# Performance work log

Measured on AMD Instinct MI355X. Metric: run time of the kernel, lower is better.

Reference implementation:

```python
import jax, jax.numpy as jnp
import numpy as np

BATCH = 8192
IN_FEATURES = 4096
OUT_FEATURES = 4096
TT_RANK = 8
IN_MODES = (16, 16, 16)
OUT_MODES = (16, 16, 16)


def setup_inputs() -> dict:
    key = jax.random.key(0)
    ks = jax.random.split(key, 5)
    # core std ~ glorot-ish scale for TT factors
    std = 0.05
    x = jax.random.normal(ks[0], (BATCH, IN_FEATURES), dtype=jnp.float32)
    core0 = std * jax.random.normal(ks[1], (1, OUT_MODES[0], IN_MODES[0], TT_RANK), dtype=jnp.float32)
    core1 = std * jax.random.normal(ks[2], (TT_RANK, OUT_MODES[1], IN_MODES[1], TT_RANK), dtype=jnp.float32)
    core2 = std * jax.random.normal(ks[3], (TT_RANK, OUT_MODES[2], IN_MODES[2], 1), dtype=jnp.float32)
    bias = 0.001 * jnp.ones((OUT_FEATURES,), dtype=jnp.float32)
    return {"x": x, "core0": core0, "core1": core1, "core2": core2, "bias": bias}


def _tt_dense_matmul(cores, b):
    """A @ b where A (out_features x in_features) is in TT-matrix format.
    cores[k]: (r_k, o_k, i_k, r_{k+1}), r_0 = r_d = 1. b: (in_features, batch).
    Returns (out_features, batch). Mirrors t3nsor/t3f tt_dense_matmul."""
    in_dims = [c.shape[2] for c in cores]
    ranks = [c.shape[0] for c in cores] + [cores[-1].shape[3]]
    out_features = int(np.prod([c.shape[1] for c in cores]))
    data = b.T                                   # (batch, in_features)
    data = data.reshape(-1, in_dims[-1], 1)      # (batch*prod(i[:-1]), i_last, r_d=1)
    for k in range(len(cores) - 1, -1, -1):
        # core (a=r_k, i=o_k, j=i_k, b=r_{k+1}); data (r, j, b) -> (i, r, a)
        data = jnp.einsum('aijb,rjb->ira', cores[k], data)
        if k > 0:
            data = data.reshape(-1, in_dims[k - 1], ranks[k])
    return data.reshape(out_features, -1)        # (out_features, batch)


def reference(x, core0, core1, core2, bias):
    # forward: tt_dense_matmul(weight_t, x^T)^T + bias
    y = _tt_dense_matmul([core0, core1, core2], x.T)  # (out_features, batch)
    return y.T + bias                                 # (batch, out_features)
```

## Files before the change

kernel.cpp:

```cpp
#include <hip/hip_runtime.h>
#include <hip/hip_bf16.h>
#include <cstdint>


typedef __bf16 bf16x8 __attribute__((ext_vector_type(8)));
typedef float f32x4 __attribute__((ext_vector_type(4)));
typedef unsigned short u16;
typedef u16 u16x8 __attribute__((ext_vector_type(8)));

__device__ __forceinline__ u16 f2bf(float f) {
    unsigned u = __builtin_bit_cast(unsigned, f);
    u += 0x7fffu + ((u >> 16) & 1u);
    return (u16)(u >> 16);
}

__global__ void k_cvt(const float* __restrict__ x, u16* __restrict__ xb) {
    long i = (long)blockIdx.x * blockDim.x + threadIdx.x;
    const float4* p = (const float4*)x;
    float4 a = p[2 * i], b = p[2 * i + 1];
    u16x8 o;
    o[0] = f2bf(a.x); o[1] = f2bf(a.y); o[2] = f2bf(a.z); o[3] = f2bf(a.w);
    o[4] = f2bf(b.x); o[5] = f2bf(b.y); o[6] = f2bf(b.z); o[7] = f2bf(b.w);
    ((u16x8*)xb)[i] = o;
}

__global__ void k_c01(const float* __restrict__ c0, const float* __restrict__ c1,
                      float* __restrict__ c01) {
    int idx = blockIdx.x * 256 + threadIdx.x;
    int b2 = idx & 7, i1 = (idx >> 3) & 15, i0 = (idx >> 7) & 15;
    int o1 = (idx >> 11) & 15, o0 = idx >> 15;
    float s = 0.f;
#pragma unroll
    for (int b1 = 0; b1 < 8; ++b1)
        s += c0[(o0 * 16 + i0) * 8 + b1] * c1[((b1 * 16 + o1) * 16 + i1) * 8 + b2];
    c01[idx] = s;
}

__global__ void k_w(const float* __restrict__ c01, const float* __restrict__ c2,
                    u16* __restrict__ wbt) {
    int idx = blockIdx.x * 256 + threadIdx.x;
    int i2h = idx & 1;
    int i1 = (idx >> 1) & 15;
    int i0 = (idx >> 5) & 15;
    int o = idx >> 9;
    int o2 = o & 15, o1 = (o >> 4) & 15, o0 = o >> 8;
    const float* c = &c01[(((o0 * 16 + o1) * 16 + i0) * 16 + i1) * 8];
    float acc[8] = {0, 0, 0, 0, 0, 0, 0, 0};
#pragma unroll
    for (int b2 = 0; b2 < 8; ++b2) {
        float cv = c[b2];
        const float* cc = &c2[(b2 * 16 + o2) * 16 + i2h * 8];
#pragma unroll
        for (int j = 0; j < 8; ++j) acc[j] += cv * cc[j];
    }
    u16x8 ov;
#pragma unroll
    for (int j = 0; j < 8; ++j) ov[j] = f2bf(acc[j]);
    ((u16x8*)wbt)[(long)o * 512 + (i0 * 32 + i1 * 2 + i2h)] = ov;
}

#define GM 128
#define GN 128
#define GK 64

__device__ __forceinline__ void gload_lds16(const void* g, void* l) {
    __builtin_amdgcn_global_load_lds(
        (const __attribute__((address_space(1))) unsigned*)g,
        (__attribute__((address_space(3))) unsigned*)l, 16, 0, 0);
}

__global__ void k_gemm(const u16* __restrict__ A, const u16* __restrict__ B,
                       const float* __restrict__ bias, float* __restrict__ C,
                       int M, int N, int K) {
    __shared__ __align__(16) u16 lA[GM * GK];
    __shared__ __align__(16) u16 lB[GN * GK];
    const int t = threadIdx.x;
    const int m0 = blockIdx.y * GM, n0 = blockIdx.x * GN;
    const int wave = t >> 6, lane = t & 63;
    const int wm = (wave >> 1) * 64, wn = (wave & 1) * 64;
    const int lr = lane & 15, quad = lane >> 4;
    const int sw = lr & 7;

    f32x4 acc[4][4];
#pragma unroll
    for (int mi = 0; mi < 4; ++mi)
#pragma unroll
        for (int ni = 0; ni < 4; ++ni) acc[mi][ni] = 0.f;

    for (int k0 = 0; k0 < K; k0 += GK) {
#pragma unroll
        for (int j = 0; j < 4; ++j) {
            int ci = j * 256 + t;
            int r = ci >> 3;
            int c = (ci & 7) ^ (r & 7);
            gload_lds16(&A[(long)(m0 + r) * K + k0 + c * 8], &lA[ci * 8]);
        }
#pragma unroll
        for (int j = 0; j < 4; ++j) {
            int ci = j * 256 + t;
            int r = ci >> 3;
            int c = (ci & 7) ^ (r & 7);
            gload_lds16(&B[(long)(n0 + r) * K + k0 + c * 8], &lB[ci * 8]);
        }
        __syncthreads();
#pragma unroll
        for (int kk2 = 0; kk2 < 2; ++kk2) {
            const int sl = ((kk2 * 4 + quad) ^ sw) * 8;
            bf16x8 af[4], bfr[4];
#pragma unroll
            for (int i = 0; i < 4; ++i)
                af[i] = *(const bf16x8*)&lA[(wm + i * 16 + lr) * GK + sl];
#pragma unroll
            for (int i = 0; i < 4; ++i)
                bfr[i] = *(const bf16x8*)&lB[(wn + i * 16 + lr) * GK + sl];
#pragma unroll
            for (int mi = 0; mi < 4; ++mi)
#pragma unroll
                for (int ni = 0; ni < 4; ++ni)
                    acc[mi][ni] = __builtin_amdgcn_mfma_f32_16x16x32_bf16(
                        af[mi], bfr[ni], acc[mi][ni], 0, 0, 0);
        }
        __syncthreads();
    }

#pragma unroll
    for (int ni = 0; ni < 4; ++ni) {
        int gn = n0 + wn + ni * 16 + lr;
        float bv = bias[gn];
#pragma unroll
        for (int mi = 0; mi < 4; ++mi) {
            int gm = m0 + wm + mi * 16 + quad * 4;
#pragma unroll
            for (int r = 0; r < 4; ++r)
                C[(long)(gm + r) * N + gn] = acc[mi][ni][r] + bv;
        }
    }
}

extern "C" void kernel_launch(void* const* d_in, const int* in_sizes, int n_in,
                              void* d_out, int out_size, void* d_ws, size_t ws_size,
                              hipStream_t stream) {
    const float* x = (const float*)d_in[0];
    const float* c0 = (const float*)d_in[1];
    const float* c1 = (const float*)d_in[2];
    const float* c2 = (const float*)d_in[3];
    const float* bias = (const float*)d_in[4];
    float* out = (float*)d_out;

    const int Mb = 8192, Nf = 4096, Kf = 4096;
    char* ws = (char*)d_ws;
    u16* xb = (u16*)ws;
    u16* wbt = (u16*)(ws + 67108864);
    float* c01 = (float*)(ws + 67108864 + 33554432);

    k_cvt<<<dim3((Mb * Kf / 8) / 256), 256, 0, stream>>>(x, xb);
    k_c01<<<dim3(2048), 256, 0, stream>>>(c0, c1, c01);
    k_w<<<dim3(8192), 256, 0, stream>>>(c01, c2, wbt);
    k_gemm<<<dim3(Nf / GN, Mb / GM), 256, 0, stream>>>(xb, wbt, bias, out, Mb, Nf, Kf);
}
```

Baseline: 476.4 us.

## Rewrite GEMM with 256x256 tiles, 4-stage LDS ring pipeline and XCD swizzle

Replaces the 128x128 single-buffered GEMM with a 256x256 tile, 8-wave workgroup that streams K in 32-wide slices through a 4-deep LDS ring of async global-to-LDS loads. Prefetches run three tiles ahead, with explicit vmcnt waits, split A/B issue, barriers and s_setprio around MFMA bursts, so that memory latency overlaps compute. A workgroup index swizzle groups tiles to improve L2 reuse. Each workgroup uses 128 KB of dynamic LDS, which limits occupancy and relies on the hand-placed waits and barriers being correct.

```diff
diff --git a/kernel.cpp b/kernel.cpp
--- a/kernel.cpp
+++ b/kernel.cpp
@@ -1,5 +1,4 @@
 #include <hip/hip_runtime.h>
-#include <hip/hip_bf16.h>
 #include <cstdint>
 
 
@@ -59,9 +58,15 @@
     ((u16x8*)wbt)[(long)o * 512 + (i0 * 32 + i1 * 2 + i2h)] = ov;
 }
 
-#define GM 128
-#define GN 128
-#define GK 64
+#define BM 256
+#define BN 256
+#define BK 32
+#define NBUF 4
+#define TA (BM * BK)
+#define TB (BN * BK)
+#define LDS_BYTES (NBUF * (TA + TB) * 2)
+
+static_assert(LDS_BYTES == 131072, "lds size");
 
 __device__ __forceinline__ void gload_lds16(const void* g, void* l) {
     __builtin_amdgcn_global_load_lds(
@@ -69,67 +74,129 @@
         (__attribute__((address_space(3))) unsigned*)l, 16, 0, 0);
 }
 
+__launch_bounds__(512, 2)
 __global__ void k_gemm(const u16* __restrict__ A, const u16* __restrict__ B,
                        const float* __restrict__ bias, float* __restrict__ C,
                        int M, int N, int K) {
-    __shared__ __align__(16) u16 lA[GM * GK];
-    __shared__ __align__(16) u16 lB[GN * GK];
+    extern __shared__ __align__(16) u16 lds[];
+    u16* lA = lds;
+    u16* lB = lds + NBUF * TA;
+
+    const int wg = blockIdx.x;
+    const int swz = (wg & 7) * 64 + (wg >> 3);
+    const int bn = swz & 15, bm = swz >> 4;
+    const int m0 = bm * BM, n0 = bn * BN;
+
     const int t = threadIdx.x;
-    const int m0 = blockIdx.y * GM, n0 = blockIdx.x * GN;
     const int wave = t >> 6, lane = t & 63;
-    const int wm = (wave >> 1) * 64, wn = (wave & 1) * 64;
+    const int wm = wave >> 2, wn = wave & 3;
     const int lr = lane & 15, quad = lane >> 4;
-    const int sw = lr & 7;
-
-    f32x4 acc[4][4];
-#pragma unroll
-    for (int mi = 0; mi < 4; ++mi)
+
+    const u16* pa[2]; const u16* pb[2]; int lof[2];
+#pragma unroll
+    for (int j = 0; j < 2; ++j) {
+        int ci = j * 512 + t;
+        int r = ci >> 2;
+        int c = (ci & 3) ^ ((r >> 1) & 3);
+        pa[j] = &A[(long)(m0 + r) * K + c * 8];
+        pb[j] = &B[(long)(n0 + r) * K + c * 8];
+        lof[j] = ci * 8;
+    }
+
+    int offA[8], offB[4];
+#pragma unroll
+    for (int mi = 0; mi < 8; ++mi) {
+        int r = wm * 128 + mi * 16 + lr;
+        offA[mi] = r * BK + ((quad ^ ((r >> 1) & 3)) << 3);
+    }
+#pragma unroll
+    for (int ni = 0; ni < 4; ++ni) {
+        int r = wn * 64 + ni * 16 + lr;
+        offB[ni] = r * BK + ((quad ^ ((r >> 1) & 3)) << 3);
+    }
+
+    f32x4 acc[8][4];
+#pragma unroll
+    for (int mi = 0; mi < 8; ++mi)
 #pragma unroll
         for (int ni = 0; ni < 4; ++ni) acc[mi][ni] = 0.f;
 
-    for (int k0 = 0; k0 < K; k0 += GK) {
-#pragma unroll
-        for (int j = 0; j < 4; ++j) {
-            int ci = j * 256 + t;
-            int r = ci >> 3;
-            int c = (ci & 7) ^ (r & 7);
-            gload_lds16(&A[(long)(m0 + r) * K + k0 + c * 8], &lA[ci * 8]);
-        }
-#pragma unroll
-        for (int j = 0; j < 4; ++j) {
-            int ci = j * 256 + t;
-            int r = ci >> 3;
-            int c = (ci & 7) ^ (r & 7);
-            gload_lds16(&B[(long)(n0 + r) * K + k0 + c * 8], &lB[ci * 8]);
-        }
-        __syncthreads();
-#pragma unroll
-        for (int kk2 = 0; kk2 < 2; ++kk2) {
-            const int sl = ((kk2 * 4 + quad) ^ sw) * 8;
-            bf16x8 af[4], bfr[4];
-#pragma unroll
-            for (int i = 0; i < 4; ++i)
-                af[i] = *(const bf16x8*)&lA[(wm + i * 16 + lr) * GK + sl];
-#pragma unroll
-            for (int i = 0; i < 4; ++i)
-                bfr[i] = *(const bf16x8*)&lB[(wn + i * 16 + lr) * GK + sl];
+    const int NT = K / BK;
+
+#pragma unroll
+    for (int tt = 0; tt < 3; ++tt) {
+#pragma unroll
+        for (int j = 0; j < 2; ++j)
+            gload_lds16(pa[j] + (long)tt * BK, lA + tt * TA + lof[j]);
+#pragma unroll
+        for (int j = 0; j < 2; ++j)
+            gload_lds16(pb[j] + (long)tt * BK, lB + tt * TB + lof[j]);
+    }
+    asm volatile("s_waitcnt vmcnt(8)" ::: "memory");
+    __builtin_amdgcn_s_barrier();
+
+#pragma unroll 1
+    for (int tb = 0; tb < NT; tb += 4) {
+#pragma unroll
+        for (int u = 0; u < 4; ++u) {
+            const int tt = tb + u;
+            const u16* aT = lA + u * TA;
+            const u16* bT = lB + u * TB;
+            const int sb = (u + 3) & 3;
+            const bool pre = (tt + 3 < NT);
+
+            if (pre) {
+#pragma unroll
+                for (int j = 0; j < 2; ++j)
+                    gload_lds16(pa[j] + (long)(tt + 3) * BK, lA + sb * TA + lof[j]);
+            }
+            bf16x8 bf[4], af[4];
+#pragma unroll
+            for (int ni = 0; ni < 4; ++ni) bf[ni] = *(const bf16x8*)&bT[offB[ni]];
+#pragma unroll
+            for (int mi = 0; mi < 4; ++mi) af[mi] = *(const bf16x8*)&aT[offA[mi]];
+            __builtin_amdgcn_s_barrier();
+            __builtin_amdgcn_s_setprio(1);
 #pragma unroll
             for (int mi = 0; mi < 4; ++mi)
 #pragma unroll
                 for (int ni = 0; ni < 4; ++ni)
                     acc[mi][ni] = __builtin_amdgcn_mfma_f32_16x16x32_bf16(
-                        af[mi], bfr[ni], acc[mi][ni], 0, 0, 0);
+                        af[mi], bf[ni], acc[mi][ni], 0, 0, 0);
+            __builtin_amdgcn_s_setprio(0);
+            __builtin_amdgcn_s_barrier();
+
+            if (pre) {
+#pragma unroll
+                for (int j = 0; j < 2; ++j)
+                    gload_lds16(pb[j] + (long)(tt + 3) * BK, lB + sb * TB + lof[j]);
+            }
+#pragma unroll
+            for (int mi = 0; mi < 4; ++mi) af[mi] = *(const bf16x8*)&aT[offA[4 + mi]];
+            __builtin_amdgcn_s_barrier();
+            __builtin_amdgcn_s_setprio(1);
+#pragma unroll
+            for (int mi = 0; mi < 4; ++mi)
+#pragma unroll
+                for (int ni = 0; ni < 4; ++ni)
+                    acc[4 + mi][ni] = __builtin_amdgcn_mfma_f32_16x16x32_bf16(
+                        af[mi], bf[ni], acc[4 + mi][ni], 0, 0, 0);
+            __builtin_amdgcn_s_setprio(0);
+
+            if (pre)                 asm volatile("s_waitcnt vmcnt(8)" ::: "memory");
+            else if (tt + 2 < NT)    asm volatile("s_waitcnt vmcnt(4)" ::: "memory");
+            else if (tt + 1 < NT)    asm volatile("s_waitcnt vmcnt(0)" ::: "memory");
+            __builtin_amdgcn_s_barrier();
         }
-        __syncthreads();
     }
 
 #pragma unroll
     for (int ni = 0; ni < 4; ++ni) {
-        int gn = n0 + wn + ni * 16 + lr;
+        int gn = n0 + wn * 64 + ni * 16 + lr;
         float bv = bias[gn];
 #pragma unroll
-        for (int mi = 0; mi < 4; ++mi) {
-            int gm = m0 + wm + mi * 16 + quad * 4;
+        for (int mi = 0; mi < 8; ++mi) {
+            int gm = m0 + wm * 128 + mi * 16 + quad * 4;
 #pragma unroll
             for (int r = 0; r < 4; ++r)
                 C[(long)(gm + r) * N + gn] = acc[mi][ni][r] + bv;
@@ -153,8 +220,12 @@
     u16* wbt = (u16*)(ws + 67108864);
     float* c01 = (float*)(ws + 67108864 + 33554432);
 
+    hipFuncSetAttribute(reinterpret_cast<const void*>(k_gemm),
+                        hipFuncAttributeMaxDynamicSharedMemorySize, LDS_BYTES);
+
     k_cvt<<<dim3((Mb * Kf / 8) / 256), 256, 0, stream>>>(x, xb);
     k_c01<<<dim3(2048), 256, 0, stream>>>(c0, c1, c01);
     k_w<<<dim3(8192), 256, 0, stream>>>(c01, c2, wbt);
-    k_gemm<<<dim3(Nf / GN, Mb / GM), 256, 0, stream>>>(xb, wbt, bias, out, Mb, Nf, Kf);
-}
+    k_gemm<<<dim3((Mb / BM) * (Nf / BN)), dim3(512), LDS_BYTES, stream>>>(
+        xb, wbt, bias, out, Mb, Nf, Kf);
+}
```

Result: slower. 489.3 us (+2.7%).

## Rewrite GEMM as 256x256 double-buffered, software-pipelined 8-wave kernel

Applied to the files above, without the earlier changes.

Replaces the 128x128 single-buffered bf16 GEMM with a 256x256 tile, 512-thread kernel. It double-buffers A/B in 128KB of dynamic LDS and interleaves global->LDS prefetch of the next K tile with quarter-tile MFMA phases, using explicit vmcnt waits, barriers and setprio. It also remaps workgroups to improve L2 locality. The aim is to hide memory latency and raise data reuse per tile, at the cost of complex hand-tuned sync, high register pressure and a hardcoded K=4096 loop count.

```diff
diff --git a/kernel.cpp b/kernel.cpp
--- a/kernel.cpp
+++ b/kernel.cpp
@@ -1,5 +1,4 @@
 #include <hip/hip_runtime.h>
-#include <hip/hip_bf16.h>
 #include <cstdint>
 
 
@@ -59,9 +58,13 @@
     ((u16x8*)wbt)[(long)o * 512 + (i0 * 32 + i1 * 2 + i2h)] = ov;
 }
 
-#define GM 128
-#define GN 128
-#define GK 64
+#define BM 256
+#define BN 256
+#define BK 64
+#define TILEU (BM * BK)
+#define LDS_BYTES (4 * TILEU * 2)
+
+static_assert(LDS_BYTES == 131072, "lds size");
 
 __device__ __forceinline__ void gload_lds16(const void* g, void* l) {
     __builtin_amdgcn_global_load_lds(
@@ -69,67 +72,132 @@
         (__attribute__((address_space(3))) unsigned*)l, 16, 0, 0);
 }
 
+#define VMW(N) asm volatile("s_waitcnt vmcnt(" #N ")" ::: "memory")
+#define LGKM0  asm volatile("s_waitcnt lgkmcnt(0)" ::: "memory")
+#define BAR()  __builtin_amdgcn_s_barrier()
+
+#define READ_A(H) do { \
+    _Pragma("unroll") for (int mi_ = 0; mi_ < 4; ++mi_) { \
+        af[mi_ * 2 + 0] = *(const bf16x8*)&aT[arow + ((H) * 128 + mi_ * 16) * 64 + swz0]; \
+        af[mi_ * 2 + 1] = *(const bf16x8*)&aT[arow + ((H) * 128 + mi_ * 16) * 64 + swz1]; \
+    } } while (0)
+
+#define READ_B(G, BF) do { \
+    _Pragma("unroll") for (int ni_ = 0; ni_ < 2; ++ni_) { \
+        BF[ni_ * 2 + 0] = *(const bf16x8*)&bT[brow + ((G) * 128 + ni_ * 16) * 64 + swz0]; \
+        BF[ni_ * 2 + 1] = *(const bf16x8*)&bT[brow + ((G) * 128 + ni_ * 16) * 64 + swz1]; \
+    } } while (0)
+
+#define MFMA16(H, G, BF) do { \
+    __builtin_amdgcn_s_setprio(1); \
+    _Pragma("unroll") for (int mi_ = 0; mi_ < 4; ++mi_) \
+    _Pragma("unroll") for (int ni_ = 0; ni_ < 2; ++ni_) \
+    _Pragma("unroll") for (int kk_ = 0; kk_ < 2; ++kk_) \
+        acc[(H) * 4 + mi_][(G) * 2 + ni_] = __builtin_amdgcn_mfma_f32_16x16x32_bf16( \
+            af[mi_ * 2 + kk_], BF[ni_ * 2 + kk_], acc[(H) * 4 + mi_][(G) * 2 + ni_], 0, 0, 0); \
+    __builtin_amdgcn_s_setprio(0); \
+} while (0)
+
+#define TILE(BUF, TT, PRE, W1, W2, W4) do { \
+    const u16* aT = lds + (BUF) * TILEU; \
+    const u16* bT = lds + 2 * TILEU + (BUF) * TILEU; \
+    u16* sA = lds + (1 - (BUF)) * TILEU; \
+    u16* sB = lds + 2 * TILEU + (1 - (BUF)) * TILEU; \
+    const long ko = (long)((TT) + 1) * BK; \
+     \
+    if (PRE) { gload_lds16(pa[0] + ko, sA + t * 8); \
+               gload_lds16(pa[1] + ko, sA + 4096 + t * 8); } \
+    READ_A(0); READ_B(0, bf0); \
+    BAR(); LGKM0; \
+    MFMA16(0, 0, bf0); \
+    W1; BAR(); \
+     \
+    if (PRE) { gload_lds16(pb[0] + ko, sB + t * 8); \
+               gload_lds16(pb[1] + ko, sB + 4096 + t * 8); } \
+    READ_B(1, bf1); \
+    BAR(); LGKM0; \
+    MFMA16(0, 1, bf1); \
+    W2; BAR(); \
+     \
+    if (PRE) { gload_lds16(pb[2] + ko, sB + 8192 + t * 8); \
+               gload_lds16(pb[3] + ko, sB + 12288 + t * 8); } \
+    READ_A(1); \
+    BAR(); LGKM0; \
+    MFMA16(1, 1, bf1); \
+    BAR(); \
+     \
+    if (PRE) { gload_lds16(pa[2] + ko, sA + 8192 + t * 8); \
+               gload_lds16(pa[3] + ko, sA + 12288 + t * 8); } \
+    MFMA16(1, 0, bf0); \
+    W4; BAR(); \
+} while (0)
+
+__launch_bounds__(512, 2)
 __global__ void k_gemm(const u16* __restrict__ A, const u16* __restrict__ B,
                        const float* __restrict__ bias, float* __restrict__ C,
                        int M, int N, int K) {
-    __shared__ __align__(16) u16 lA[GM * GK];
-    __shared__ __align__(16) u16 lB[GN * GK];
+    extern __shared__ __align__(16) u16 lds[];
+
+    const int wg = blockIdx.x;
+    const int swzb = (wg & 7) * 64 + (wg >> 3);
+    const int bn = swzb & 15, bm = swzb >> 4;
+    const int m0 = bm * BM, n0 = bn * BN;
+
     const int t = threadIdx.x;
-    const int m0 = blockIdx.y * GM, n0 = blockIdx.x * GN;
     const int wave = t >> 6, lane = t & 63;
-    const int wm = (wave >> 1) * 64, wn = (wave & 1) * 64;
+    const int wm = wave >> 2, wn = wave & 3;
     const int lr = lane & 15, quad = lane >> 4;
-    const int sw = lr & 7;
-
-    f32x4 acc[4][4];
-#pragma unroll
-    for (int mi = 0; mi < 4; ++mi)
+
+    const u16 *pa[4], *pb[4];
+#pragma unroll
+    for (int j = 0; j < 4; ++j) {
+        int ci = j * 512 + t;
+        int lrow = ci >> 3;
+        int c = (ci & 7) ^ (lrow & 7);
+        int rA = ((lrow >> 6) & 1) * 128 + (lrow >> 7) * 64 + (lrow & 63);
+        int rB = ((lrow >> 5) & 3) * 64 + (lrow >> 7) * 32 + (lrow & 31);
+        pa[j] = &A[(long)(m0 + rA) * K + c * 8];
+        pb[j] = &B[(long)(n0 + rB) * K + c * 8];
+    }
+
+    const int swz0 = ((quad    ) ^ (lr & 7)) * 8;
+    const int swz1 = ((quad + 4) ^ (lr & 7)) * 8;
+    const int arow = (wm * 64 + lr) * 64;
+    const int brow = (wn * 32 + lr) * 64;
+
+    f32x4 acc[8][4];
+#pragma unroll
+    for (int mi = 0; mi < 8; ++mi)
 #pragma unroll
         for (int ni = 0; ni < 4; ++ni) acc[mi][ni] = 0.f;
 
-    for (int k0 = 0; k0 < K; k0 += GK) {
-#pragma unroll
-        for (int j = 0; j < 4; ++j) {
-            int ci = j * 256 + t;
-            int r = ci >> 3;
-            int c = (ci & 7) ^ (r & 7);
-            gload_lds16(&A[(long)(m0 + r) * K + k0 + c * 8], &lA[ci * 8]);
-        }
-#pragma unroll
-        for (int j = 0; j < 4; ++j) {
-            int ci = j * 256 + t;
-            int r = ci >> 3;
-            int c = (ci & 7) ^ (r & 7);
-            gload_lds16(&B[(long)(n0 + r) * K + k0 + c * 8], &lB[ci * 8]);
-        }
-        __syncthreads();
-#pragma unroll
-        for (int kk2 = 0; kk2 < 2; ++kk2) {
-            const int sl = ((kk2 * 4 + quad) ^ sw) * 8;
-            bf16x8 af[4], bfr[4];
-#pragma unroll
-            for (int i = 0; i < 4; ++i)
-                af[i] = *(const bf16x8*)&lA[(wm + i * 16 + lr) * GK + sl];
-#pragma unroll
-            for (int i = 0; i < 4; ++i)
-                bfr[i] = *(const bf16x8*)&lB[(wn + i * 16 + lr) * GK + sl];
-#pragma unroll
-            for (int mi = 0; mi < 4; ++mi)
-#pragma unroll
-                for (int ni = 0; ni < 4; ++ni)
-                    acc[mi][ni] = __builtin_amdgcn_mfma_f32_16x16x32_bf16(
-                        af[mi], bfr[ni], acc[mi][ni], 0, 0, 0);
-        }
-        __syncthreads();
-    }
+    bf16x8 af[8], bf0[4], bf1[4];
+
+    gload_lds16(pa[0], lds + t * 8);
+    gload_lds16(pa[1], lds + 4096 + t * 8);
+    gload_lds16(pb[0], lds + 2 * TILEU + t * 8);
+    gload_lds16(pb[1], lds + 2 * TILEU + 4096 + t * 8);
+    gload_lds16(pb[2], lds + 2 * TILEU + 8192 + t * 8);
+    gload_lds16(pb[3], lds + 2 * TILEU + 12288 + t * 8);
+    gload_lds16(pa[2], lds + 8192 + t * 8);
+    gload_lds16(pa[3], lds + 12288 + t * 8);
+    VMW(4); BAR();
+
+#pragma unroll 1
+    for (int tt = 0; tt < 62; tt += 2) {
+        TILE(0, tt,     1, VMW(4), VMW(4), VMW(4));
+        TILE(1, tt + 1, 1, VMW(4), VMW(4), VMW(4));
+    }
+    TILE(0, 62, 1, VMW(4), VMW(4), VMW(4));
+    TILE(1, 63, 0, VMW(2), VMW(0), );
 
 #pragma unroll
     for (int ni = 0; ni < 4; ++ni) {
-        int gn = n0 + wn + ni * 16 + lr;
+        int gn = n0 + wn * 64 + ni * 16 + lr;
         float bv = bias[gn];
 #pragma unroll
-        for (int mi = 0; mi < 4; ++mi) {
-            int gm = m0 + wm + mi * 16 + quad * 4;
+        for (int mi = 0; mi < 8; ++mi) {
+            int gm = m0 + wm * 128 + mi * 16 + quad * 4;
 #pragma unroll
             for (int r = 0; r < 4; ++r)
                 C[(long)(gm + r) * N + gn] = acc[mi][ni][r] + bv;
@@ -153,8 +221,12 @@
     u16* wbt = (u16*)(ws + 67108864);
     float* c01 = (float*)(ws + 67108864 + 33554432);
 
+    hipFuncSetAttribute(reinterpret_cast<const void*>(k_gemm),
+                        hipFuncAttributeMaxDynamicSharedMemorySize, LDS_BYTES);
+
     k_cvt<<<dim3((Mb * Kf / 8) / 256), 256, 0, stream>>>(x, xb);
     k_c01<<<dim3(2048), 256, 0, stream>>>(c0, c1, c01);
     k_w<<<dim3(8192), 256, 0, stream>>>(c01, c2, wbt);
-    k_gemm<<<dim3(Nf / GN, Mb / GM), 256, 0, stream>>>(xb, wbt, bias, out, Mb, Nf, Kf);
-}
+    k_gemm<<<dim3((Mb / BM) * (Nf / BN)), dim3(512), LDS_BYTES, stream>>>(
+        xb, wbt, bias, out, Mb, Nf, Kf);
+}
```

Measured after the change: 464.5 us. 2.5% less time.

## Rewrite GEMM with 256x256 tiles, double-buffered LDS and 32x32 MFMA

Applied to the files above, without the earlier changes.

The bf16 GEMM is rebuilt around 256x256 block tiles and 8 waves per block, using 32x32x16 MFMA instructions in place of 16x16x32. LDS is double-buffered (128 KB dynamic), and global-to-LDS loads for the next K tile are interleaved with MFMA work on the current one. Manual waitcnt, sched_barrier and setprio calls control the schedule, and the 1D grid is swizzled so neighbouring blocks share data in L2. This targets the single-buffered load-sync-compute stalls of the old kernel, at the cost of heavy register pressure, large LDS use that limits occupancy, and hardcoded dimensions.

```diff
diff --git a/kernel.cpp b/kernel.cpp
--- a/kernel.cpp
+++ b/kernel.cpp
@@ -1,10 +1,9 @@
 #include <hip/hip_runtime.h>
-#include <hip/hip_bf16.h>
 #include <cstdint>
 
 
 typedef __bf16 bf16x8 __attribute__((ext_vector_type(8)));
-typedef float f32x4 __attribute__((ext_vector_type(4)));
+typedef float f32x16 __attribute__((ext_vector_type(16)));
 typedef unsigned short u16;
 typedef u16 u16x8 __attribute__((ext_vector_type(8)));
 
@@ -59,9 +58,10 @@
     ((u16x8*)wbt)[(long)o * 512 + (i0 * 32 + i1 * 2 + i2h)] = ov;
 }
 
-#define GM 128
-#define GN 128
-#define GK 64
+#define BM 256
+#define BN 256
+#define BK 64
+#define LDS_BYTES 131072
 
 __device__ __forceinline__ void gload_lds16(const void* g, void* l) {
     __builtin_amdgcn_global_load_lds(
@@ -69,70 +69,118 @@
         (__attribute__((address_space(3))) unsigned*)l, 16, 0, 0);
 }
 
+#define VMW(N)  asm volatile("s_waitcnt vmcnt(" #N ")" ::: "memory")
+#define LGKM(N) asm volatile("s_waitcnt lgkmcnt(" #N ")" ::: "memory")
+#define BAR()   __builtin_amdgcn_s_barrier()
+#define SCHED0  __builtin_amdgcn_sched_barrier(0)
+
+#define READ6(KS, AF, BF, BUF) do { \
+    _Pragma("unroll") for (int mi_ = 0; mi_ < 4; ++mi_) \
+        AF[mi_] = *(const bf16x8*)(ldsb + vA[KS] + ((BUF) * 32768 + mi_ * 4096)); \
+    _Pragma("unroll") for (int ni_ = 0; ni_ < 2; ++ni_) \
+        BF[ni_] = *(const bf16x8*)(ldsb + vB[KS] + ((BUF) * 32768 + ni_ * 4096)); \
+} while (0)
+
+#define MFMA8(AF, BF) do { \
+    __builtin_amdgcn_s_setprio(1); \
+    _Pragma("unroll") for (int mi_ = 0; mi_ < 4; ++mi_) \
+    _Pragma("unroll") for (int ni_ = 0; ni_ < 2; ++ni_) \
+        acc[mi_][ni_] = __builtin_amdgcn_mfma_f32_32x32x16_bf16( \
+            AF[mi_], BF[ni_], acc[mi_][ni_], 0, 0, 0); \
+    __builtin_amdgcn_s_setprio(0); \
+} while (0)
+
+#define GLOADA(G, DSTBUF, KO) \
+    gload_lds16(paT + (long)(G) * 64 * 4096 + (KO), \
+                ldsw + (DSTBUF) * 32768 + (G) * 8192 + t * 16)
+#define GLOADB(G, DSTBUF, KO) \
+    gload_lds16(pbT + (long)(G) * 64 * 4096 + (KO), \
+                ldsw + 65536 + (DSTBUF) * 32768 + (G) * 8192 + t * 16)
+
+#define TILE(BUF, TT, PRE) do { \
+    const long ko_ = (long)((TT) + 1) * BK; \
+    READ6(0, a0, b0, BUF); \
+    READ6(1, a1, b1, BUF); \
+    LGKM(6); SCHED0; \
+    MFMA8(a0, b0); \
+    if (PRE) { GLOADA(0, 1 - (BUF), ko_); GLOADA(1, 1 - (BUF), ko_); \
+               GLOADA(2, 1 - (BUF), ko_); GLOADA(3, 1 - (BUF), ko_); } \
+    READ6(2, a0, b0, BUF); \
+    LGKM(6); SCHED0; \
+    MFMA8(a1, b1); \
+    if (PRE) { GLOADB(0, 1 - (BUF), ko_); GLOADB(1, 1 - (BUF), ko_); \
+               GLOADB(2, 1 - (BUF), ko_); GLOADB(3, 1 - (BUF), ko_); } \
+    READ6(3, a1, b1, BUF); \
+    LGKM(6); SCHED0; \
+    MFMA8(a0, b0); \
+    LGKM(0); SCHED0; \
+    MFMA8(a1, b1); \
+    VMW(0); BAR(); \
+} while (0)
+
+__launch_bounds__(512, 2)
 __global__ void k_gemm(const u16* __restrict__ A, const u16* __restrict__ B,
                        const float* __restrict__ bias, float* __restrict__ C,
                        int M, int N, int K) {
-    __shared__ __align__(16) u16 lA[GM * GK];
-    __shared__ __align__(16) u16 lB[GN * GK];
+    extern __shared__ __align__(16) u16 lds[];
+    char* ldsw = (char*)lds;
+    const char* ldsb = (const char*)lds;
+
+    const int wg = blockIdx.x;
+    const int swzb = (wg & 7) * 64 + (wg >> 3);
+    const int bn = swzb & 15, bm = swzb >> 4;
+    const int m0 = bm * BM, n0 = bn * BN;
+
     const int t = threadIdx.x;
-    const int m0 = blockIdx.y * GM, n0 = blockIdx.x * GN;
     const int wave = t >> 6, lane = t & 63;
-    const int wm = (wave >> 1) * 64, wn = (wave & 1) * 64;
-    const int lr = lane & 15, quad = lane >> 4;
-    const int sw = lr & 7;
-
-    f32x4 acc[4][4];
+    const int wm = wave >> 2, wn = wave & 3;
+    const int l31 = lane & 31, hi = lane >> 5, l7 = lane & 7;
+
+    const int srow = t >> 3;
+    const int sc = (t & 7) ^ (srow & 7);
+    const u16* paT = A + (long)m0 * K + (long)srow * K + sc * 8;
+    const u16* pbT = B + (long)n0 * K + (long)srow * K + sc * 8;
+
+    int vA[4], vB[4];
+#pragma unroll
+    for (int ks = 0; ks < 4; ++ks) {
+        int so = ((2 * ks + hi) ^ l7) << 4;
+        vA[ks] = wm * 16384 + l31 * 128 + so;
+        vB[ks] = 65536 + wn * 8192 + l31 * 128 + so;
+    }
+
+    f32x16 acc[4][2];
 #pragma unroll
     for (int mi = 0; mi < 4; ++mi)
 #pragma unroll
-        for (int ni = 0; ni < 4; ++ni) acc[mi][ni] = 0.f;
-
-    for (int k0 = 0; k0 < K; k0 += GK) {
-#pragma unroll
-        for (int j = 0; j < 4; ++j) {
-            int ci = j * 256 + t;
-            int r = ci >> 3;
-            int c = (ci & 7) ^ (r & 7);
-            gload_lds16(&A[(long)(m0 + r) * K + k0 + c * 8], &lA[ci * 8]);
-        }
-#pragma unroll
-        for (int j = 0; j < 4; ++j) {
-            int ci = j * 256 + t;
-            int r = ci >> 3;
-            int c = (ci & 7) ^ (r & 7);
-            gload_lds16(&B[(long)(n0 + r) * K + k0 + c * 8], &lB[ci * 8]);
-        }
-        __syncthreads();
-#pragma unroll
-        for (int kk2 = 0; kk2 < 2; ++kk2) {
-            const int sl = ((kk2 * 4 + quad) ^ sw) * 8;
-            bf16x8 af[4], bfr[4];
-#pragma unroll
-            for (int i = 0; i < 4; ++i)
-                af[i] = *(const bf16x8*)&lA[(wm + i * 16 + lr) * GK + sl];
-#pragma unroll
-            for (int i = 0; i < 4; ++i)
-                bfr[i] = *(const bf16x8*)&lB[(wn + i * 16 + lr) * GK + sl];
-#pragma unroll
-            for (int mi = 0; mi < 4; ++mi)
-#pragma unroll
-                for (int ni = 0; ni < 4; ++ni)
-                    acc[mi][ni] = __builtin_amdgcn_mfma_f32_16x16x32_bf16(
-                        af[mi], bfr[ni], acc[mi][ni], 0, 0, 0);
-        }
-        __syncthreads();
-    }
-
-#pragma unroll
-    for (int ni = 0; ni < 4; ++ni) {
-        int gn = n0 + wn + ni * 16 + lr;
+        for (int ni = 0; ni < 2; ++ni) acc[mi][ni] = 0.f;
+
+    bf16x8 a0[4], a1[4], b0[2], b1[2];
+
+    GLOADA(0, 0, 0); GLOADA(1, 0, 0); GLOADA(2, 0, 0); GLOADA(3, 0, 0);
+    GLOADB(0, 0, 0); GLOADB(1, 0, 0); GLOADB(2, 0, 0); GLOADB(3, 0, 0);
+    VMW(0); BAR();
+
+#pragma unroll 1
+    for (int tt = 0; tt < 62; tt += 2) {
+        TILE(0, tt,     1);
+        TILE(1, tt + 1, 1);
+    }
+    TILE(0, 62, 1);
+    TILE(1, 63, 0);
+
+#pragma unroll
+    for (int ni = 0; ni < 2; ++ni) {
+        int gn = n0 + wn * 64 + ni * 32 + l31;
         float bv = bias[gn];
 #pragma unroll
         for (int mi = 0; mi < 4; ++mi) {
-            int gm = m0 + wm + mi * 16 + quad * 4;
-#pragma unroll
-            for (int r = 0; r < 4; ++r)
-                C[(long)(gm + r) * N + gn] = acc[mi][ni][r] + bv;
+            int gm = m0 + wm * 128 + mi * 32 + 4 * hi;
+#pragma unroll
+            for (int reg = 0; reg < 16; ++reg) {
+                int r = (reg & 3) + 8 * (reg >> 2);
+                C[(long)(gm + r) * N + gn] = acc[mi][ni][reg] + bv;
+            }
         }
     }
 }
@@ -153,8 +201,12 @@
     u16* wbt = (u16*)(ws + 67108864);
     float* c01 = (float*)(ws + 67108864 + 33554432);
 
+    hipFuncSetAttribute(reinterpret_cast<const void*>(k_gemm),
+                        hipFuncAttributeMaxDynamicSharedMemorySize, LDS_BYTES);
+
     k_cvt<<<dim3((Mb * Kf / 8) / 256), 256, 0, stream>>>(x, xb);
     k_c01<<<dim3(2048), 256, 0, stream>>>(c0, c1, c01);
     k_w<<<dim3(8192), 256, 0, stream>>>(c01, c2, wbt);
-    k_gemm<<<dim3(Nf / GN, Mb / GM), 256, 0, stream>>>(xb, wbt, bias, out, Mb, Nf, Kf);
-}
+    k_gemm<<<dim3((Mb / BM) * (Nf / BN)), dim3(512), LDS_BYTES, stream>>>(
+        xb, wbt, bias, out, Mb, Nf, Kf);
+}
```

After: 483.7 us. About the same (+1.5%).
